# Kernel optimization log

Hardware: AMD Instinct MI355X
Metric: run time of the kernel (lower is better)

## Reference

```python
import jax, jax.numpy as jnp
import numpy as np

T, B, IN, H, E = 100, 1, 36, 256, 2048


def setup_inputs() -> dict:
    key = jax.random.key(0)
    ks = jax.random.split(key, 18)
    rn = lambda k, shape, s=1.0: jax.random.normal(k, shape, jnp.float32) * s
    return dict(
        Y=rn(ks[0], (T, B, IN)),
        h0=rn(ks[1], (1, B, H)),
        c0=rn(ks[2], (1, B, H)),
        outEncoder=rn(ks[3], (E, H), 0.1),
        W_ih=rn(ks[4], (4 * H, IN), 0.1),
        W_hh=rn(ks[5], (4 * H, H), 0.1),
        b_ih=rn(ks[6], (4 * H,), 0.1),
        b_hh=rn(ks[7], (4 * H,), 0.1),
        att_W=rn(ks[8], (H, H), 0.1),
        att_V=rn(ks[9], (H, H), 0.1),
        att_b=rn(ks[10], (H, 1), 0.1),
        att_vector=rn(ks[11], (1, H), 0.1),
        W1=rn(ks[12], (H, 2 * H), 0.1),
        b1=rn(ks[13], (H,), 0.1),
        W2=rn(ks[14], (H, H), 0.1),
        b2=rn(ks[15], (H,), 0.1),
        W3=rn(ks[16], (IN, H), 0.1),
        b3=rn(ks[17], (IN,), 0.1),
    )


def reference(Y, h0, c0, outEncoder, W_ih, W_hh, b_ih, b_hh,
              att_W, att_V, att_b, att_vector, W1, b1, W2, b2, W3, b3):
    h = jnp.squeeze(h0, 0)  # [B,H]
    c = jnp.squeeze(c0, 0)  # [B,H]
    # VOut = att_V @ outEncoder^T is timestep-invariant: precompute. [H,E]
    VOut = att_V @ outEncoder.T

    def step(carry, y):
        h, c = carry  # h: [B,H], c: [B,H] (context from prev step after step 0)
        gates = y @ W_ih.T + b_ih + h @ W_hh.T + b_hh  # [B,4H]
        i_g, f_g, g_g, o_g = jnp.split(gates, 4, axis=1)
        cLSTM = jax.nn.sigmoid(f_g) * c + jax.nn.sigmoid(i_g) * jnp.tanh(g_g)
        h_new = jax.nn.sigmoid(o_g) * jnp.tanh(cLSTM)  # [B,H]
        # additive attention: hidden expanded to every encoder position
        WS = att_W @ h_new.T  # [H,1], broadcasts over E columns
        Escore = jnp.tanh(WS + VOut + att_b)  # [H,E]
        scores = att_vector @ Escore  # [1,E]
        alpha = jax.nn.softmax(scores, axis=-1)  # [1,E]
        ctx = alpha @ outEncoder  # [1,H]
        # MLP on concat(new cell state, context)
        v = jnp.concatenate([cLSTM, ctx], axis=1)  # [1,2H]
        v = jax.nn.relu(v @ W1.T + b1)
        v = jax.nn.relu(v @ W2.T + b2)
        out = v @ W3.T + b3  # [1,36]
        # NB: original feeds the attention context back as the LSTM cell state
        return (h_new, ctx), out

    (_, c_final), outputs = jax.lax.scan(step, (h, c), Y)
    return outputs, c_final  # outputs: [100,1,36]
```

## Files before the change

### kernel.cpp

```cpp
#include <hip/hip_runtime.h>
#include <stdint.h>


static constexpr float    L2E = 1.44269504088896341f;
static constexpr float    K2  = 2.88539008177792681f;
static constexpr unsigned SPIN_LIMIT = 200000u;

static constexpr size_t OFF_BC   = 0;
static constexpr size_t OFF_YG   = 524288;
static constexpr size_t OFF_GRAW = 626688;
static constexpr size_t OFF_CRAW = 729088;
static constexpr size_t OFF_STOT = 754688;
static constexpr size_t OFF_CLH  = 754816;
static constexpr size_t OFF_V1   = 780416;
static constexpr size_t OFF_V2   = 806016;
static constexpr size_t OFF_SYNC = 831616;

__device__ __forceinline__ float exp2fast(float x){ return __builtin_amdgcn_exp2f(x); }
__device__ __forceinline__ float rcpfast(float x){ return __builtin_amdgcn_rcpf(x); }
__device__ __forceinline__ float sigf(float x){ return rcpfast(1.f + exp2fast(-x*L2E)); }
__device__ __forceinline__ float tanhfast(float x){
  float E = exp2fast(x*K2);
  return 1.f - 2.f*rcpfast(E + 1.f);
}
__device__ __forceinline__ unsigned short f2bf(float f){
  unsigned b = __float_as_uint(f);
  return (unsigned short)((b + 0x7FFFu + ((b>>16)&1u))>>16);
}
__device__ __forceinline__ float bf2f(unsigned short u){ return __uint_as_float(((unsigned)u)<<16); }

__device__ __forceinline__ void gstore(float* p, float v){
  __hip_atomic_store(p, v, __ATOMIC_RELAXED, __HIP_MEMORY_SCOPE_AGENT);
}
__device__ __forceinline__ float gload(const float* p){
  return __hip_atomic_load(p, __ATOMIC_RELAXED, __HIP_MEMORY_SCOPE_AGENT);
}
__device__ __forceinline__ void gstore_u32(unsigned* p, unsigned v){
  __hip_atomic_store(p, v, __ATOMIC_RELAXED, __HIP_MEMORY_SCOPE_AGENT);
}
__device__ __forceinline__ unsigned gload_u32(const unsigned* p){
  return __hip_atomic_load(p, __ATOMIC_RELAXED, __HIP_MEMORY_SCOPE_AGENT);
}
__device__ __forceinline__ void gatomic_addf(float* p, float v){
  (void)__hip_atomic_fetch_add(p, v, __ATOMIC_RELAXED, __HIP_MEMORY_SCOPE_AGENT);
}

__device__ __forceinline__ void fbar(unsigned* flags, int w, unsigned ep){
  asm volatile("s_waitcnt vmcnt(0)" ::: "memory");
  __syncthreads();
  if (threadIdx.x == 0) gstore_u32(&flags[w], ep);
  if (threadIdx.x < 64) {
    int lane = threadIdx.x;
    unsigned it = 0;
    for (;;) {
      unsigned v = (lane < 32) ? gload_u32(&flags[lane]) : ep;
      if (__all((int)(v >= ep))) break;
      if (++it > SPIN_LIMIT) break;
    }
  }
  __syncthreads();
}
__device__ __forceinline__ void fwait_sleep(unsigned* flags, unsigned ep){
  if (threadIdx.x < 64) {
    int lane = threadIdx.x;
    unsigned it = 0;
    for (;;) {
      unsigned v = (lane < 32) ? gload_u32(&flags[lane]) : ep;
      if (__all((int)(v >= ep))) break;
      __builtin_amdgcn_s_sleep(2);
      if (++it > SPIN_LIMIT) break;
    }
  }
  __syncthreads();
}
__device__ __forceinline__ void arrive_cnt(unsigned* cnt){
  asm volatile("s_waitcnt vmcnt(0)" ::: "memory");
  __syncthreads();
  if (threadIdx.x == 0)
    __hip_atomic_fetch_add(cnt, 1u, __ATOMIC_RELAXED, __HIP_MEMORY_SCOPE_AGENT);
}
__device__ __forceinline__ void poll_ge(unsigned* p, unsigned tgt){
  if (threadIdx.x == 0){
    unsigned it = 0;
    while (gload_u32(p) < tgt){
      __builtin_amdgcn_s_sleep(2);
      if (++it > SPIN_LIMIT) break;
    }
  }
  __syncthreads();
}

__global__ __launch_bounds__(256) void rnn_prep(
    const float* __restrict__ Y, const float* __restrict__ h0,
    const float* __restrict__ outE, const float* __restrict__ W_ih,
    const float* __restrict__ W_hh, const float* __restrict__ b_ih,
    const float* __restrict__ b_hh, const float* __restrict__ att_V,
    const float* __restrict__ att_b, float* __restrict__ ws)
{
  __shared__ float avT[32*257];
  __shared__ float oeL[8*257];
  __shared__ float yL[40];
  __shared__ float h0L[256];
  const int b = blockIdx.x, tid = threadIdx.x;
  float* ws_bc   = ws + OFF_BC;
  float* ws_yg   = ws + OFF_YG;
  float* ws_graw = ws + OFF_GRAW;

  if (b < 256) {
    int e0 = b*8;
    for (int r=0;r<8;r++) oeL[r*257 + tid] = outE[(size_t)(e0+r)*256 + tid];
    int hl = tid & 31, er = tid >> 5;
    for (int ht=0; ht<8; ++ht) {
      __syncthreads();
      for (int i=0;i<32;i++){ int lin = tid + i*256; int r = lin>>8, j = lin&255;
        avT[r*257 + j] = att_V[(size_t)(ht*32+r)*256 + j]; }
      __syncthreads();
      float acc = 0.f;
      for (int j=0;j<256;j++) acc = fmaf(avT[hl*257 + j], oeL[er*257 + j], acc);
      int h = ht*32 + hl;
      ws_bc[(size_t)(e0+er)*256 + h] = (acc + att_b[h]) * K2;
    }
  } else if (b < 260) {
    int g = b - 256;
    for (int u=0; u<25; ++u) {
      int t = g*25 + u;
      __syncthreads();
      if (tid < 36) yL[tid] = Y[t*36 + tid];
      __syncthreads();
      for (int q=0;q<4;q++){
        int i = tid + 256*q;
        float acc = b_ih[i] + b_hh[i];
        for (int j=0;j<36;j++) acc = fmaf(W_ih[(size_t)i*36 + j], yL[j], acc);
        ws_yg[(size_t)t*1024 + i] = acc;
      }
    }
  } else if (b < 292) {
    int s = b - 260;
    if (tid < 256) h0L[tid] = h0[tid];
    if (tid < 36)  yL[tid]  = Y[tid];
    __syncthreads();
    int r = tid>>3, l8 = tid&7;
    int R = s*32 + r;
    float acc = 0.f;
    for (int q=0;q<32;q++){ int j = l8*32 + q; acc = fmaf(W_hh[(size_t)R*256 + j], h0L[j], acc); }
    acc += __shfl_xor(acc,1); acc += __shfl_xor(acc,2); acc += __shfl_xor(acc,4);
    if (l8 == 0){
      float full = acc + b_ih[R] + b_hh[R];
      for (int j=0;j<36;j++) full = fmaf(W_ih[(size_t)R*36 + j], yL[j], full);
      ws_graw[R] = full;
    }
  } else if (b == 292) {
    unsigned* s0 = (unsigned*)(ws + OFF_SYNC);
    s0[tid] = 0u; s0[tid + 256] = 0u;
  } else if (b == 293) {
    if (tid < 128) ws[OFF_STOT + tid] = 0.f;
  } else {
    int t = b - 294;
    ws[OFF_CRAW + (size_t)t*256 + tid] = 0.f;
  }
}

__global__ __launch_bounds__(512, 2) void rnn_main(
    const float* __restrict__ c0, const float* __restrict__ outE,
    const float* __restrict__ W_hh, const float* __restrict__ att_W,
    const float* __restrict__ att_vec,
    const float* __restrict__ W1, const float* __restrict__ b1,
    const float* __restrict__ W2, const float* __restrict__ b2,
    const float* __restrict__ W3, const float* __restrict__ b3,
    float* __restrict__ out, float* __restrict__ ws)
{
  __shared__ __align__(16) unsigned char smem[140288];
  const int w = blockIdx.x;
  const int tid = threadIdx.x;

  float* ws_yg   = ws + OFF_YG;
  float* ws_graw = ws + OFF_GRAW;
  float* ws_craw = ws + OFF_CRAW;
  float* ws_stot = ws + OFF_STOT;
  float* ws_clh  = ws + OFF_CLH;
  float* ws_v1   = ws + OFF_V1;
  float* ws_v2   = ws + OFF_V2;
  unsigned* flags = (unsigned*)(ws + OFF_SYNC);
  unsigned* fv1   = flags + 64;
  unsigned* fv2   = flags + 192;

  if (w < 32) {
    float*          bcS    = (float*)(smem);
    unsigned short* oeS    = (unsigned short*)(smem + 67584);
    float*          whhS   = (float*)(smem + 100352);
    float*          wsS    = (float*)(smem + 133632);
    float*          hS     = (float*)(smem + 134688);
    float*          scoreS = (float*)(smem + 135712);
    float*          wexpS  = (float*)(smem + 135968);
    float*          pS     = (float*)(smem + 136224);
    float*          avS    = (float*)(smem + 138272);

    float awR[128];
    { int r = tid>>1, p = tid&1;
      const float* arow = att_W + (size_t)r*256 + p*128;
      #pragma unroll
      for (int q=0;q<128;q++) awR[q] = arow[q]; }
    float Vpart = 0.f;
    { int l8 = tid & 7;
      #pragma unroll
      for (int k=0;k<32;k++) Vpart += att_vec[l8*32 + k]; }

    const float* ws_bc = ws + OFF_BC;
    for (int i=0;i<32;i++){ int lin = tid + i*512; int col = lin>>8, h = lin&255;
      bcS[col*264 + h + (h>>5)] = ws_bc[(size_t)(w*64+col)*256 + h]; }
    for (int i=0;i<32;i++){ int lin = tid + i*512; int col = lin>>8, h = lin&255;
      oeS[col*256 + h] = f2bf(outE[(size_t)(w*64+col)*256 + h]); }
    for (int i=0;i<16;i++){ int lin = tid + i*512; int r = lin>>8, j = lin&255;
      whhS[r*260 + j] = W_hh[(size_t)(w*32+r)*256 + j]; }
    if (tid < 256) avS[tid + (tid>>5)] = -2.f * att_vec[tid];
    __syncthreads();

    for (int t = 0; t < 100; ++t) {
      if (tid < 256) {
        float c;
        if (t == 0) c = c0[tid];
        else {
          float raw = gload(&ws_craw[(size_t)(t-1)*256 + tid]);
          float st  = gload(&ws_stot[t-1]);
          c = raw * rcpfast(st);
        }
        const float* g = ws_graw + (size_t)t*1024;
        float ig = gload(&g[tid]),     fg = gload(&g[256+tid]);
        float gg = gload(&g[512+tid]), og = gload(&g[768+tid]);
        float cl = sigf(fg)*c + sigf(ig)*tanhfast(gg);
        float hn = sigf(og)*tanhfast(cl);
        hS[tid] = hn;
        if (w == 0) gstore(&ws_clh[(size_t)t*256 + tid], cl);
      }
      __syncthreads();
      { int r = tid>>1, p = tid&1;
        const float4* h4 = (const float4*)(hS + p*128);
        float acc = 0.f;
        #pragma unroll
        for (int i=0;i<32;i++){ float4 hv = h4[i];
          acc = fmaf(awR[4*i+0], hv.x, acc);
          acc = fmaf(awR[4*i+1], hv.y, acc);
          acc = fmaf(awR[4*i+2], hv.z, acc);
          acc = fmaf(awR[4*i+3], hv.w, acc); }
        acc += __shfl_xor(acc, 1);
        if (p == 0) wsS[r + (r>>5)] = acc * K2; }
      __syncthreads();
      { int col = tid >> 3, l8 = tid & 7;
        const float* bcR = bcS + col*264 + l8*33;
        const float* wsR = wsS + l8*33;
        const float* avR = avS + l8*33;
        float acc = Vpart;
        #pragma unroll
        for (int k=0;k<32;k++){
          float E = exp2fast(bcR[k] + wsR[k]);
          acc = fmaf(avR[k], rcpfast(E + 1.f), acc);
        }
        acc += __shfl_xor(acc,1); acc += __shfl_xor(acc,2); acc += __shfl_xor(acc,4);
        if (l8 == 0) scoreS[col] = acc; }
      __syncthreads();
      if (tid < 64) {
        float ev = exp2fast(scoreS[tid] * L2E);
        wexpS[tid] = ev;
        float s = ev;
        #pragma unroll
        for (int d=1; d<64; d<<=1) s += __shfl_xor(s, d);
        if (tid == 0) gatomic_addf(&ws_stot[t], s);
      }
      __syncthreads();
      { int h = tid & 255, half = tid >> 8;
        float accp = 0.f;
        #pragma unroll
        for (int i=0;i<32;i++){ int lc = half*32 + i;
          accp = fmaf(wexpS[lc], bf2f(oeS[lc*256 + h]), accp); }
        pS[half*256 + h] = accp; }
      __syncthreads();
      if (tid < 256) gatomic_addf(&ws_craw[(size_t)t*256 + tid], pS[tid] + pS[256 + tid]);
      if (t <= 98) {
        int r32 = tid >> 4, l16 = tid & 15;
        float acc2 = 0.f;
        #pragma unroll
        for (int q=0;q<16;q++){ int j = l16 + 16*q; acc2 = fmaf(whhS[r32*260 + j], hS[j], acc2); }
        acc2 += __shfl_xor(acc2,1); acc2 += __shfl_xor(acc2,2);
        acc2 += __shfl_xor(acc2,4); acc2 += __shfl_xor(acc2,8);
        if (l16 == 0){ int R = w*32 + r32;
          gstore(&ws_graw[(size_t)(t+1)*1024 + R], acc2 + ws_yg[(size_t)(t+1)*1024 + R]); }
      }
      fbar(flags, w, (unsigned)(t+1));
    }
    if (w == 0 && tid < 256) {
      float raw = gload(&ws_craw[(size_t)99*256 + tid]);
      float st  = gload(&ws_stot[99]);
      out[3600 + tid] = raw * rcpfast(st);
    }
  } else if (w < 36) {
    float* wmS = (float*)(smem);
    float* vbS = (float*)(smem + 133632);
    int m = w - 32;
    for (int i=0;i<64;i++){ int lin = tid + i*512; int r = lin>>9, k = lin&511;
      wmS[r*520 + k + (k>>6)] = W1[(size_t)(m*64+r)*512 + k]; }
    __syncthreads();
    for (int s=0; s<100; ++s){
      fwait_sleep(flags, (unsigned)(s+1));
      { float val;
        if (tid < 256) val = gload(&ws_clh[(size_t)s*256 + tid]);
        else { float raw = gload(&ws_craw[(size_t)s*256 + (tid-256)]);
               float st  = gload(&ws_stot[s]);
               val = raw * rcpfast(st); }
        vbS[tid + (tid>>6)] = val; }
      __syncthreads();
      int row = tid >> 3, l8 = tid & 7;
      const float* wr = wmS + row*520 + l8*65;
      const float* vr = vbS + l8*65;
      float acc = 0.f;
      #pragma unroll
      for (int q=0;q<64;q++) acc = fmaf(wr[q], vr[q], acc);
      acc += __shfl_xor(acc,1); acc += __shfl_xor(acc,2); acc += __shfl_xor(acc,4);
      if (l8 == 0){ int i = m*64 + row; gstore(&ws_v1[(size_t)s*256 + i], fmaxf(acc + b1[i], 0.f)); }
      arrive_cnt(&fv1[s]);
    }
  } else if (w < 38) {
    float* wmS = (float*)(smem);
    float* vbS = (float*)(smem + 133632);
    int m = w - 36;
    for (int i=0;i<64;i++){ int lin = tid + i*512; int r = lin>>8, k = lin&255;
      wmS[r*260 + k + (k>>6)] = W2[(size_t)(m*128+r)*256 + k]; }
    __syncthreads();
    for (int s=0; s<100; ++s){
      poll_ge(&fv1[s], 4u);
      if (tid < 256) vbS[tid + (tid>>6)] = gload(&ws_v1[(size_t)s*256 + tid]);
      __syncthreads();
      int row = tid >> 2, l4 = tid & 3;
      const float* wr = wmS + row*260 + l4*65;
      const float* vr = vbS + l4*65;
      float acc = 0.f;
      #pragma unroll
      for (int q=0;q<64;q++) acc = fmaf(wr[q], vr[q], acc);
      acc += __shfl_xor(acc,1); acc += __shfl_xor(acc,2);
      if (l4 == 0){ int i = m*128 + row; gstore(&ws_v2[(size_t)s*256 + i], fmaxf(acc + b2[i], 0.f)); }
      arrive_cnt(&fv2[s]);
      __syncthreads();
    }
  } else {
    float* wmS = (float*)(smem);
    float* vbS = (float*)(smem + 37440);
    for (int lin = tid; lin < 36*256; lin += 512){ int r = lin>>8, k = lin&255;
      wmS[r*260 + k + (k>>6)] = W3[(size_t)r*256 + k]; }
    __syncthreads();
    for (int s=0; s<100; ++s){
      poll_ge(&fv2[s], 2u);
      if (tid < 256) vbS[tid + (tid>>6)] = gload(&ws_v2[(size_t)s*256 + tid]);
      __syncthreads();
      if (tid < 288) {
        int row = tid >> 3, l8 = tid & 7;
        int kb = l8*32;
        const float* wr = wmS + row*260 + kb + (kb>>6);
        const float* vr = vbS + kb + (kb>>6);
        float acc = 0.f;
        #pragma unroll
        for (int q=0;q<32;q++) acc = fmaf(wr[q], vr[q], acc);
        acc += __shfl_xor(acc,1); acc += __shfl_xor(acc,2); acc += __shfl_xor(acc,4);
        if (l8 == 0) out[s*36 + row] = acc + b3[row];
      }
      __syncthreads();
    }
  }
}

extern "C" void kernel_launch(void* const* d_in, const int* in_sizes, int n_in,
                              void* d_out, int out_size, void* d_ws, size_t ws_size,
                              hipStream_t stream) {
  (void)in_sizes; (void)n_in; (void)out_size; (void)ws_size;
  const float* Y       = (const float*)d_in[0];
  const float* h0      = (const float*)d_in[1];
  const float* c0      = (const float*)d_in[2];
  const float* outEnc  = (const float*)d_in[3];
  const float* W_ih    = (const float*)d_in[4];
  const float* W_hh    = (const float*)d_in[5];
  const float* b_ih    = (const float*)d_in[6];
  const float* b_hh    = (const float*)d_in[7];
  const float* att_W   = (const float*)d_in[8];
  const float* att_V   = (const float*)d_in[9];
  const float* att_b   = (const float*)d_in[10];
  const float* att_vec = (const float*)d_in[11];
  const float* W1      = (const float*)d_in[12];
  const float* b1      = (const float*)d_in[13];
  const float* W2      = (const float*)d_in[14];
  const float* b2      = (const float*)d_in[15];
  const float* W3      = (const float*)d_in[16];
  const float* b3      = (const float*)d_in[17];
  float* out = (float*)d_out;
  float* ws  = (float*)d_ws;

  rnn_prep<<<dim3(394), dim3(256), 0, stream>>>(Y, h0, outEnc, W_ih, W_hh, b_ih, b_hh,
                                                att_V, att_b, ws);
  rnn_main<<<dim3(39), dim3(512), 0, stream>>>(c0, outEnc, W_hh, att_W, att_vec,
                                               W1, b1, W2, b2, W3, b3, out, ws);
}
```

Before: 722.5 us.

## Spread softmax and context atomics into per-block partial slots with plain loads

The softmax denominator is no longer accumulated with one float atomic per block into a single address. Each block writes its partial sum to its own slot, and consumers reduce the 32 slots with a wave shuffle. The context accumulation is split into 8 partial lanes per element, chosen by block group, to reduce contention on the same atomic address; readers sum those 8 lanes with two float4 loads. Atomic relaxed loads are replaced with plain loads plus compiler memory barriers after the spin waits, the att_W register preload is vectorised, and the clh stores are spread across blocks. Launch bounds drop to one block per SM. Plain loads from global memory risk visibility problems if the hardware caches are not coherent at that point.

Result: slower. 767.1 us (+6.2%).

```diff
diff --git a/kernel.cpp b/kernel.cpp
--- a/kernel.cpp
+++ b/kernel.cpp
@@ -10,11 +10,11 @@
 static constexpr size_t OFF_YG   = 524288;
 static constexpr size_t OFF_GRAW = 626688;
 static constexpr size_t OFF_CRAW = 729088;
-static constexpr size_t OFF_STOT = 754688;
-static constexpr size_t OFF_CLH  = 754816;
-static constexpr size_t OFF_V1   = 780416;
-static constexpr size_t OFF_V2   = 806016;
-static constexpr size_t OFF_SYNC = 831616;
+static constexpr size_t OFF_STOT = 933888;
+static constexpr size_t OFF_CLH  = 937088;
+static constexpr size_t OFF_V1   = 962688;
+static constexpr size_t OFF_V2   = 988288;
+static constexpr size_t OFF_SYNC = 1013888;
 
 __device__ __forceinline__ float exp2fast(float x){ return __builtin_amdgcn_exp2f(x); }
 __device__ __forceinline__ float rcpfast(float x){ return __builtin_amdgcn_rcpf(x); }
@@ -31,9 +31,6 @@
 
 __device__ __forceinline__ void gstore(float* p, float v){
   __hip_atomic_store(p, v, __ATOMIC_RELAXED, __HIP_MEMORY_SCOPE_AGENT);
-}
-__device__ __forceinline__ float gload(const float* p){
-  return __hip_atomic_load(p, __ATOMIC_RELAXED, __HIP_MEMORY_SCOPE_AGENT);
 }
 __device__ __forceinline__ void gstore_u32(unsigned* p, unsigned v){
   __hip_atomic_store(p, v, __ATOMIC_RELAXED, __HIP_MEMORY_SCOPE_AGENT);
@@ -59,6 +56,7 @@
     }
   }
   __syncthreads();
+  asm volatile("" ::: "memory");
 }
 __device__ __forceinline__ void fwait_sleep(unsigned* flags, unsigned ep){
   if (threadIdx.x < 64) {
@@ -72,6 +70,7 @@
     }
   }
   __syncthreads();
+  asm volatile("" ::: "memory");
 }
 __device__ __forceinline__ void arrive_cnt(unsigned* cnt){
   asm volatile("s_waitcnt vmcnt(0)" ::: "memory");
@@ -88,6 +87,7 @@
     }
   }
   __syncthreads();
+  asm volatile("" ::: "memory");
 }
 
 __global__ __launch_bounds__(256) void rnn_prep(
@@ -153,14 +153,14 @@
     unsigned* s0 = (unsigned*)(ws + OFF_SYNC);
     s0[tid] = 0u; s0[tid + 256] = 0u;
   } else if (b == 293) {
-    if (tid < 128) ws[OFF_STOT + tid] = 0.f;
+    for (int k=0;k<13;k++){ int i = tid + k*256; if (i < 3200) ws[OFF_STOT + i] = 0.f; }
   } else {
     int t = b - 294;
-    ws[OFF_CRAW + (size_t)t*256 + tid] = 0.f;
+    for (int k=0;k<8;k++) ws[OFF_CRAW + (size_t)t*2048 + tid + k*256] = 0.f;
   }
 }
 
-__global__ __launch_bounds__(512, 2) void rnn_main(
+__global__ __launch_bounds__(512, 1) void rnn_main(
     const float* __restrict__ c0, const float* __restrict__ outE,
     const float* __restrict__ W_hh, const float* __restrict__ att_W,
     const float* __restrict__ att_vec,
@@ -173,13 +173,13 @@
   const int w = blockIdx.x;
   const int tid = threadIdx.x;
 
-  float* ws_yg   = ws + OFF_YG;
-  float* ws_graw = ws + OFF_GRAW;
-  float* ws_craw = ws + OFF_CRAW;
-  float* ws_stot = ws + OFF_STOT;
-  float* ws_clh  = ws + OFF_CLH;
-  float* ws_v1   = ws + OFF_V1;
-  float* ws_v2   = ws + OFF_V2;
+  float* ws_yg    = ws + OFF_YG;
+  float* ws_graw  = ws + OFF_GRAW;
+  float* ws_craw  = ws + OFF_CRAW;
+  float* ws_stotp = ws + OFF_STOT;
+  float* ws_clh   = ws + OFF_CLH;
+  float* ws_v1    = ws + OFF_V1;
+  float* ws_v2    = ws + OFF_V2;
   unsigned* flags = (unsigned*)(ws + OFF_SYNC);
   unsigned* fv1   = flags + 64;
   unsigned* fv2   = flags + 192;
@@ -194,12 +194,13 @@
     float*          wexpS  = (float*)(smem + 135968);
     float*          pS     = (float*)(smem + 136224);
     float*          avS    = (float*)(smem + 138272);
-
-    float awR[128];
+    float*          stS    = (float*)(smem + 139328);
+
+    float4 awR[32];
     { int r = tid>>1, p = tid&1;
-      const float* arow = att_W + (size_t)r*256 + p*128;
+      const float4* arow = (const float4*)(att_W + (size_t)r*256 + p*128);
       #pragma unroll
-      for (int q=0;q<128;q++) awR[q] = arow[q]; }
+      for (int q=0;q<32;q++) awR[q] = arow[q]; }
     float Vpart = 0.f;
     { int l8 = tid & 7;
       #pragma unroll
@@ -216,32 +217,43 @@
     __syncthreads();
 
     for (int t = 0; t < 100; ++t) {
+      float ig, fg, gg, og;
+      float4 cv0, cv1;
+      if (tid < 256) {
+        const float* g = ws_graw + (size_t)t*1024;
+        ig = g[tid]; fg = g[256+tid]; gg = g[512+tid]; og = g[768+tid];
+        if (t > 0) {
+          const float4* cp = (const float4*)(ws_craw + ((size_t)(t-1)*256 + tid)*8);
+          cv0 = cp[0]; cv1 = cp[1];
+        }
+      }
+      if (t > 0 && tid < 64) {
+        float v = (tid < 32) ? ws_stotp[(size_t)(t-1)*32 + tid] : 0.f;
+        #pragma unroll
+        for (int d=1; d<64; d<<=1) v += __shfl_xor(v, d);
+        if (tid == 0) stS[0] = v;
+      }
+      __syncthreads();
       if (tid < 256) {
         float c;
         if (t == 0) c = c0[tid];
         else {
-          float raw = gload(&ws_craw[(size_t)(t-1)*256 + tid]);
-          float st  = gload(&ws_stot[t-1]);
-          c = raw * rcpfast(st);
+          float rsum = (cv0.x+cv0.y)+(cv0.z+cv0.w) + (cv1.x+cv1.y)+(cv1.z+cv1.w);
+          c = rsum * rcpfast(stS[0]);
         }
-        const float* g = ws_graw + (size_t)t*1024;
-        float ig = gload(&g[tid]),     fg = gload(&g[256+tid]);
-        float gg = gload(&g[512+tid]), og = gload(&g[768+tid]);
         float cl = sigf(fg)*c + sigf(ig)*tanhfast(gg);
         float hn = sigf(og)*tanhfast(cl);
         hS[tid] = hn;
-        if (w == 0) gstore(&ws_clh[(size_t)t*256 + tid], cl);
+        if ((tid>>3) == w) gstore(&ws_clh[(size_t)t*256 + tid], cl);
       }
       __syncthreads();
       { int r = tid>>1, p = tid&1;
         const float4* h4 = (const float4*)(hS + p*128);
         float acc = 0.f;
         #pragma unroll
-        for (int i=0;i<32;i++){ float4 hv = h4[i];
-          acc = fmaf(awR[4*i+0], hv.x, acc);
-          acc = fmaf(awR[4*i+1], hv.y, acc);
-          acc = fmaf(awR[4*i+2], hv.z, acc);
-          acc = fmaf(awR[4*i+3], hv.w, acc); }
+        for (int i=0;i<32;i++){ float4 hv = h4[i]; float4 av = awR[i];
+          acc = fmaf(av.x, hv.x, acc); acc = fmaf(av.y, hv.y, acc);
+          acc = fmaf(av.z, hv.z, acc); acc = fmaf(av.w, hv.w, acc); }
         acc += __shfl_xor(acc, 1);
         if (p == 0) wsS[r + (r>>5)] = acc * K2; }
       __syncthreads();
@@ -264,7 +276,7 @@
         float s = ev;
         #pragma unroll
         for (int d=1; d<64; d<<=1) s += __shfl_xor(s, d);
-        if (tid == 0) gatomic_addf(&ws_stot[t], s);
+        if (tid == 0) gstore(&ws_stotp[(size_t)t*32 + w], s);
       }
       __syncthreads();
       { int h = tid & 255, half = tid >> 8;
@@ -274,7 +286,8 @@
           accp = fmaf(wexpS[lc], bf2f(oeS[lc*256 + h]), accp); }
         pS[half*256 + h] = accp; }
       __syncthreads();
-      if (tid < 256) gatomic_addf(&ws_craw[(size_t)t*256 + tid], pS[tid] + pS[256 + tid]);
+      if (tid < 256)
+        gatomic_addf(&ws_craw[((size_t)t*256 + tid)*8 + (w>>2)], pS[tid] + pS[256 + tid]);
       if (t <= 98) {
         int r32 = tid >> 4, l16 = tid & 15;
         float acc2 = 0.f;
@@ -287,25 +300,47 @@
       }
       fbar(flags, w, (unsigned)(t+1));
     }
-    if (w == 0 && tid < 256) {
-      float raw = gload(&ws_craw[(size_t)99*256 + tid]);
-      float st  = gload(&ws_stot[99]);
-      out[3600 + tid] = raw * rcpfast(st);
+    if (w == 0) {
+      if (tid < 64) {
+        float v = (tid < 32) ? ws_stotp[(size_t)99*32 + tid] : 0.f;
+        #pragma unroll
+        for (int d=1; d<64; d<<=1) v += __shfl_xor(v, d);
+        if (tid == 0) stS[0] = v;
+      }
+      __syncthreads();
+      if (tid < 256) {
+        const float4* cp = (const float4*)(ws_craw + ((size_t)99*256 + tid)*8);
+        float4 a = cp[0], b = cp[1];
+        float rsum = (a.x+a.y)+(a.z+a.w) + (b.x+b.y)+(b.z+b.w);
+        out[3600 + tid] = rsum * rcpfast(stS[0]);
+      }
     }
   } else if (w < 36) {
-    float* wmS = (float*)(smem);
-    float* vbS = (float*)(smem + 133632);
+    float* wmS  = (float*)(smem);
+    float* vbS  = (float*)(smem + 133632);
+    float* stSm = (float*)(smem + 136000);
     int m = w - 32;
     for (int i=0;i<64;i++){ int lin = tid + i*512; int r = lin>>9, k = lin&511;
       wmS[r*520 + k + (k>>6)] = W1[(size_t)(m*64+r)*512 + k]; }
     __syncthreads();
     for (int s=0; s<100; ++s){
       fwait_sleep(flags, (unsigned)(s+1));
-      { float val;
-        if (tid < 256) val = gload(&ws_clh[(size_t)s*256 + tid]);
-        else { float raw = gload(&ws_craw[(size_t)s*256 + (tid-256)]);
-               float st  = gload(&ws_stot[s]);
-               val = raw * rcpfast(st); }
+      if (tid < 64) {
+        float v = (tid < 32) ? ws_stotp[(size_t)s*32 + tid] : 0.f;
+        #pragma unroll
+        for (int d=1; d<64; d<<=1) v += __shfl_xor(v, d);
+        if (tid == 0) stSm[0] = v;
+      }
+      float rawsum = 0.f;
+      if (tid >= 256) {
+        int h = tid - 256;
+        const float4* cp = (const float4*)(ws_craw + ((size_t)s*256 + h)*8);
+        float4 a = cp[0], b = cp[1];
+        rawsum = (a.x+a.y)+(a.z+a.w) + (b.x+b.y)+(b.z+b.w);
+      }
+      __syncthreads();
+      { float val = (tid < 256) ? ws_clh[(size_t)s*256 + tid]
+                                : rawsum * rcpfast(stSm[0]);
         vbS[tid + (tid>>6)] = val; }
       __syncthreads();
       int row = tid >> 3, l8 = tid & 7;
@@ -317,6 +352,7 @@
       acc += __shfl_xor(acc,1); acc += __shfl_xor(acc,2); acc += __shfl_xor(acc,4);
       if (l8 == 0){ int i = m*64 + row; gstore(&ws_v1[(size_t)s*256 + i], fmaxf(acc + b1[i], 0.f)); }
       arrive_cnt(&fv1[s]);
+      __syncthreads();
     }
   } else if (w < 38) {
     float* wmS = (float*)(smem);
@@ -327,7 +363,7 @@
     __syncthreads();
     for (int s=0; s<100; ++s){
       poll_ge(&fv1[s], 4u);
-      if (tid < 256) vbS[tid + (tid>>6)] = gload(&ws_v1[(size_t)s*256 + tid]);
+      if (tid < 256) vbS[tid + (tid>>6)] = ws_v1[(size_t)s*256 + tid];
       __syncthreads();
       int row = tid >> 2, l4 = tid & 3;
       const float* wr = wmS + row*260 + l4*65;
@@ -348,7 +384,7 @@
     __syncthreads();
     for (int s=0; s<100; ++s){
       poll_ge(&fv2[s], 2u);
-      if (tid < 256) vbS[tid + (tid>>6)] = gload(&ws_v2[(size_t)s*256 + tid]);
+      if (tid < 256) vbS[tid + (tid>>6)] = ws_v2[(size_t)s*256 + tid];
       __syncthreads();
       if (tid < 288) {
         int row = tid >> 3, l8 = tid & 7;
```

## Split context atomics into four partial copies and pack att_W as bf16

Applied to the files above, without the earlier changes.

The context accumulator now has four separate copies, one per group of eight worker blocks. This is meant to cut contention on the global float atomics, and readers sum the four partials. att_W rows held in registers are packed as bf16 pairs, halving register use, and the gate and context loads are hoisted ahead of the compute. It also adds a __syncthreads in the W1 loop and uses atomic stores for init. The cost is lower att_W precision and extra loads per reader.

After: 680.6 us. -5.8%, faster.

```diff
diff --git a/kernel.cpp b/kernel.cpp
--- a/kernel.cpp
+++ b/kernel.cpp
@@ -10,11 +10,12 @@
 static constexpr size_t OFF_YG   = 524288;
 static constexpr size_t OFF_GRAW = 626688;
 static constexpr size_t OFF_CRAW = 729088;
-static constexpr size_t OFF_STOT = 754688;
-static constexpr size_t OFF_CLH  = 754816;
-static constexpr size_t OFF_V1   = 780416;
-static constexpr size_t OFF_V2   = 806016;
-static constexpr size_t OFF_SYNC = 831616;
+static constexpr size_t CRAW_CP  = 25600;
+static constexpr size_t OFF_STOT = 831488;
+static constexpr size_t OFF_CLH  = 831616;
+static constexpr size_t OFF_V1   = 857216;
+static constexpr size_t OFF_V2   = 882816;
+static constexpr size_t OFF_SYNC = 908416;
 
 __device__ __forceinline__ float exp2fast(float x){ return __builtin_amdgcn_exp2f(x); }
 __device__ __forceinline__ float rcpfast(float x){ return __builtin_amdgcn_rcpf(x); }
@@ -151,12 +152,14 @@
     }
   } else if (b == 292) {
     unsigned* s0 = (unsigned*)(ws + OFF_SYNC);
-    s0[tid] = 0u; s0[tid + 256] = 0u;
+    gstore_u32(&s0[tid], 0u); gstore_u32(&s0[tid + 256], 0u);
   } else if (b == 293) {
-    if (tid < 128) ws[OFF_STOT + tid] = 0.f;
+    if (tid < 128) gstore(&ws[OFF_STOT + tid], 0.f);
   } else {
     int t = b - 294;
-    ws[OFF_CRAW + (size_t)t*256 + tid] = 0.f;
+    #pragma unroll
+    for (int c=0;c<4;c++)
+      gstore(&ws[OFF_CRAW + (size_t)c*CRAW_CP + (size_t)t*256 + tid], 0.f);
   }
 }
 
@@ -173,13 +176,13 @@
   const int w = blockIdx.x;
   const int tid = threadIdx.x;
 
-  float* ws_yg   = ws + OFF_YG;
-  float* ws_graw = ws + OFF_GRAW;
-  float* ws_craw = ws + OFF_CRAW;
-  float* ws_stot = ws + OFF_STOT;
-  float* ws_clh  = ws + OFF_CLH;
-  float* ws_v1   = ws + OFF_V1;
-  float* ws_v2   = ws + OFF_V2;
+  float* ws_yg    = ws + OFF_YG;
+  float* ws_graw  = ws + OFF_GRAW;
+  float* ws_craw  = ws + OFF_CRAW;
+  float* ws_stot  = ws + OFF_STOT;
+  float* ws_clh   = ws + OFF_CLH;
+  float* ws_v1    = ws + OFF_V1;
+  float* ws_v2    = ws + OFF_V2;
   unsigned* flags = (unsigned*)(ws + OFF_SYNC);
   unsigned* fv1   = flags + 64;
   unsigned* fv2   = flags + 192;
@@ -194,12 +197,17 @@
     float*          wexpS  = (float*)(smem + 135968);
     float*          pS     = (float*)(smem + 136224);
     float*          avS    = (float*)(smem + 138272);
-
-    float awR[128];
+    float*          stS    = (float*)(smem + 139328);
+
+    unsigned awP[64];
     { int r = tid>>1, p = tid&1;
       const float* arow = att_W + (size_t)r*256 + p*128;
       #pragma unroll
-      for (int q=0;q<128;q++) awR[q] = arow[q]; }
+      for (int q=0;q<64;q++){
+        unsigned lo = f2bf(arow[2*q]);
+        unsigned hi = f2bf(arow[2*q+1]);
+        awP[q] = lo | (hi<<16);
+      } }
     float Vpart = 0.f;
     { int l8 = tid & 7;
       #pragma unroll
@@ -216,17 +224,23 @@
     __syncthreads();
 
     for (int t = 0; t < 100; ++t) {
+      float ig, fg, gg, og;
+      float cr0, cr1, cr2, cr3, st;
+      if (tid < 256) {
+        const float* g = ws_graw + (size_t)t*1024;
+        ig = gload(&g[tid]);     fg = gload(&g[256+tid]);
+        gg = gload(&g[512+tid]); og = gload(&g[768+tid]);
+        if (t > 0) {
+          const float* cb = ws_craw + (size_t)(t-1)*256 + tid;
+          cr0 = gload(cb);             cr1 = gload(cb + CRAW_CP);
+          cr2 = gload(cb + 2*CRAW_CP); cr3 = gload(cb + 3*CRAW_CP);
+          st  = gload(&ws_stot[t-1]);
+        }
+      }
       if (tid < 256) {
         float c;
         if (t == 0) c = c0[tid];
-        else {
-          float raw = gload(&ws_craw[(size_t)(t-1)*256 + tid]);
-          float st  = gload(&ws_stot[t-1]);
-          c = raw * rcpfast(st);
-        }
-        const float* g = ws_graw + (size_t)t*1024;
-        float ig = gload(&g[tid]),     fg = gload(&g[256+tid]);
-        float gg = gload(&g[512+tid]), og = gload(&g[768+tid]);
+        else        c = ((cr0+cr1)+(cr2+cr3)) * rcpfast(st);
         float cl = sigf(fg)*c + sigf(ig)*tanhfast(gg);
         float hn = sigf(og)*tanhfast(cl);
         hS[tid] = hn;
@@ -237,11 +251,14 @@
         const float4* h4 = (const float4*)(hS + p*128);
         float acc = 0.f;
         #pragma unroll
-        for (int i=0;i<32;i++){ float4 hv = h4[i];
-          acc = fmaf(awR[4*i+0], hv.x, acc);
-          acc = fmaf(awR[4*i+1], hv.y, acc);
-          acc = fmaf(awR[4*i+2], hv.z, acc);
-          acc = fmaf(awR[4*i+3], hv.w, acc); }
+        for (int i=0;i<32;i++){
+          float4 hv = h4[i];
+          unsigned pk0 = awP[2*i], pk1 = awP[2*i+1];
+          acc = fmaf(__uint_as_float(pk0<<16),          hv.x, acc);
+          acc = fmaf(__uint_as_float(pk0 & 0xffff0000u), hv.y, acc);
+          acc = fmaf(__uint_as_float(pk1<<16),          hv.z, acc);
+          acc = fmaf(__uint_as_float(pk1 & 0xffff0000u), hv.w, acc);
+        }
         acc += __shfl_xor(acc, 1);
         if (p == 0) wsS[r + (r>>5)] = acc * K2; }
       __syncthreads();
@@ -274,7 +291,9 @@
           accp = fmaf(wexpS[lc], bf2f(oeS[lc*256 + h]), accp); }
         pS[half*256 + h] = accp; }
       __syncthreads();
-      if (tid < 256) gatomic_addf(&ws_craw[(size_t)t*256 + tid], pS[tid] + pS[256 + tid]);
+      if (tid < 256)
+        gatomic_addf(&ws_craw[(size_t)(w>>3)*CRAW_CP + (size_t)t*256 + tid],
+                     pS[tid] + pS[256 + tid]);
       if (t <= 98) {
         int r32 = tid >> 4, l16 = tid & 15;
         float acc2 = 0.f;
@@ -288,9 +307,10 @@
       fbar(flags, w, (unsigned)(t+1));
     }
     if (w == 0 && tid < 256) {
-      float raw = gload(&ws_craw[(size_t)99*256 + tid]);
-      float st  = gload(&ws_stot[99]);
-      out[3600 + tid] = raw * rcpfast(st);
+      const float* cb = ws_craw + (size_t)99*256 + tid;
+      float rsum = (gload(cb) + gload(cb + CRAW_CP))
+                 + (gload(cb + 2*CRAW_CP) + gload(cb + 3*CRAW_CP));
+      out[3600 + tid] = rsum * rcpfast(gload(&ws_stot[99]));
     }
   } else if (w < 36) {
     float* wmS = (float*)(smem);
@@ -303,9 +323,12 @@
       fwait_sleep(flags, (unsigned)(s+1));
       { float val;
         if (tid < 256) val = gload(&ws_clh[(size_t)s*256 + tid]);
-        else { float raw = gload(&ws_craw[(size_t)s*256 + (tid-256)]);
-               float st  = gload(&ws_stot[s]);
-               val = raw * rcpfast(st); }
+        else {
+          const float* cb = ws_craw + (size_t)s*256 + (tid-256);
+          float rsum = (gload(cb) + gload(cb + CRAW_CP))
+                     + (gload(cb + 2*CRAW_CP) + gload(cb + 3*CRAW_CP));
+          val = rsum * rcpfast(gload(&ws_stot[s]));
+        }
         vbS[tid + (tid>>6)] = val; }
       __syncthreads();
       int row = tid >> 3, l8 = tid & 7;
@@ -317,6 +340,7 @@
       acc += __shfl_xor(acc,1); acc += __shfl_xor(acc,2); acc += __shfl_xor(acc,4);
       if (l8 == 0){ int i = m*64 + row; gstore(&ws_v1[(size_t)s*256 + i], fmaxf(acc + b1[i], 0.f)); }
       arrive_cnt(&fv1[s]);
+      __syncthreads();
     }
   } else if (w < 38) {
     float* wmS = (float*)(smem);
```
